# Kernel tuning notes

Measured on AMD Instinct MI355X. Metric: run time of the kernel, lower is better.

## Reference

```python
import jax, jax.numpy as jnp
import numpy as np
from jax import lax

GAIN = 16.0           # encoder_gains[0]
TEMP = 0.3            # soft_round_temperature
MASK = 9              # mask_size
PAD = 4               # (MASK - 1) // 2
# dim_arm = 16 causal taps inside the 9x9 mask (all indices < center index 40)
CTX_IDX = [12, 13, 14, 20, 21, 22, 23, 24, 28, 29, 30, 31, 32, 33, 38, 39]
CTX_OFF = [(i // MASK, i % MASK) for i in CTX_IDX]
IMG_H, IMG_W = 1024, 1536
N_GRIDS = 7
SIZES = [(int(np.ceil(IMG_H / 2 ** i)), int(np.ceil(IMG_W / 2 ** i))) for i in range(N_GRIDS)]
N_TOTAL = sum(h * w for h, w in SIZES)  # 2097024


def _softround(x, t):
    fl = jnp.floor(x)
    return fl + 0.5 * jnp.tanh((x - fl - 0.5) / t) / jnp.tanh(0.5 / t) + 0.5


def _forward(latents, noise_u, arm_w1, arm_b1, arm_w2, arm_b2, arm_wo, arm_bo,
             ups_k, pre_k, syn_w1, syn_b1, syn_w2, syn_b2):
    # --- quantize latents: softround(softround(x*g) + kumaraswamy noise), a=1 -> uniform-0.5 ---
    flat = jnp.concatenate([l.reshape(-1) for l in latents]) * GAIN
    flat_q = _softround(_softround(flat, TEMP) + (noise_u - 0.5), TEMP)
    dec, cnt = [], 0
    for h, w in SIZES:
        dec.append(flat_q[cnt:cnt + h * w].reshape(1, 1, h, w))
        cnt += h * w
    # --- _get_neighbor: masked causal context gather (16 taps of the 9x9 mask) ---
    ctxs = []
    for l in dec:
        h, w = l.shape[2], l.shape[3]
        xp = jnp.pad(l[0, 0], PAD)  # zero pad, matches F.pad constant 0
        ctxs.append(jnp.stack([xp[dy:dy + h, dx:dx + w] for dy, dx in CTX_OFF], axis=-1).reshape(-1, len(CTX_OFF)))
    ctx = jnp.concatenate(ctxs, axis=0)  # [N, 16]
    # --- ARM MLP: residual hidden layers, final linear to (mu, log_scale) ---
    h1 = jax.nn.relu(ctx @ arm_w1.T + arm_b1 + ctx)
    h2 = jax.nn.relu(h1 @ arm_w2.T + arm_b2 + h1)
    raw = h2 @ arm_wo.T + arm_bo
    mu, log_s = raw[:, 0], raw[:, 1]
    scale = jnp.exp(-0.5 * jnp.clip(log_s, -13.8155, 13.8155))
    def lcdf(x):
        return 0.5 - 0.5 * jnp.sign(x - mu) * jnp.expm1(-jnp.abs(x - mu) / scale)
    proba = jnp.maximum(lcdf(flat_q + 0.5) - lcdf(flat_q - 0.5), 2.0 ** -16)
    rate = -jnp.log2(proba)
    # --- upsampling: coarse-to-fine, depthwise separable convT x2 + preconcat filter ---
    x = dec[-1]
    for step, i in enumerate(range(N_GRIDS - 1, 0, -1)):
        c = x.shape[1]
        kern = jnp.broadcast_to(jnp.outer(ups_k[step], ups_k[step])[None, None], (c, 1, 8, 8))
        x = lax.conv_general_dilated(x, kern, (1, 1), ((4, 4), (4, 4)), lhs_dilation=(2, 2),
                                     dimension_numbers=('NCHW', 'OIHW', 'NCHW'), feature_group_count=c)
        ht, wt = SIZES[i - 1]
        x = x[:, :, :ht, :wt]
        pk2 = jnp.outer(pre_k[step], pre_k[step])[None, None]  # (1,1,7,7)
        t = lax.conv_general_dilated(dec[i - 1], pk2, (1, 1), ((3, 3), (3, 3)),
                                     dimension_numbers=('NCHW', 'OIHW', 'NCHW'))
        x = jnp.concatenate([t, x], axis=1)
    # --- synthesis: 1x1 conv 7->48 relu, 48->6, split mean / log_scale ---
    hid = jax.nn.relu(jnp.einsum('bchw,oc->bohw', x, syn_w1) + syn_b1[None, :, None, None])
    out = jnp.einsum('bchw,oc->bohw', hid, syn_w2) + syn_b2[None, :, None, None]
    pixel_mean, pixel_log_scale = out[:, :3], out[:, 3:]
    # F.interpolate to img_size is identity here (already full resolution)
    decoded = jnp.clip(pixel_mean, 0.0, 1.0)
    return pixel_mean, pixel_log_scale, decoded, rate


def setup_inputs():
    key = jax.random.key(0)
    ks = jax.random.split(key, 16)
    d = {}
    for i, (h, w) in enumerate(SIZES):
        d['latent%d' % i] = jax.random.uniform(ks[i], (1, 1, h, w), jnp.float32, -0.5, 0.5)
    d['noise_u'] = jax.random.uniform(ks[7], (N_TOTAL,), jnp.float32)
    d['arm_w1'] = jax.random.normal(ks[8], (16, 16), jnp.float32) * 0.25
    d['arm_b1'] = jnp.zeros((16,), jnp.float32)
    d['arm_w2'] = jax.random.normal(ks[9], (16, 16), jnp.float32) * 0.25
    d['arm_b2'] = jnp.zeros((16,), jnp.float32)
    d['arm_wo'] = jax.random.normal(ks[10], (2, 16), jnp.float32) * 0.25
    d['arm_bo'] = jnp.zeros((2,), jnp.float32)
    d['ups_k'] = jax.random.normal(ks[11], (6, 8), jnp.float32) * 0.2 + 0.125
    d['pre_k'] = jax.random.normal(ks[12], (6, 7), jnp.float32) * 0.2 + 0.1
    d['syn_w1'] = jax.random.normal(ks[13], (48, 7), jnp.float32) * 0.3
    d['syn_b1'] = jnp.zeros((48,), jnp.float32)
    d['syn_w2'] = jax.random.normal(ks[14], (6, 48), jnp.float32) * 0.1
    d['syn_b2'] = jnp.zeros((6,), jnp.float32)
    return d


def reference(latent0, latent1, latent2, latent3, latent4, latent5, latent6, noise_u,
              arm_w1, arm_b1, arm_w2, arm_b2, arm_wo, arm_bo,
              ups_k, pre_k, syn_w1, syn_b1, syn_w2, syn_b2):
    return _forward([latent0, latent1, latent2, latent3, latent4, latent5, latent6], noise_u,
                    arm_w1, arm_b1, arm_w2, arm_b2, arm_wo, arm_bo,
                    ups_k, pre_k, syn_w1, syn_b1, syn_w2, syn_b2)
```

## Files before the change

kernel.cpp:

```cpp
#include <hip/hip_runtime.h>
#include <math.h>

#define N_TOTAL 2097024
#define HWF (1024 * 1536)

#define OFF0 0
#define OFF1 1572864
#define OFF2 1966080
#define OFF3 2064384
#define OFF4 2088960
#define OFF5 2095104
#define OFF6 2096640

#define OUT_LS   (3 * HWF)
#define OUT_DEC  (6 * HWF)
#define OUT_RATE (9 * HWF)

typedef float f4 __attribute__((ext_vector_type(4), aligned(4)));
typedef float f2 __attribute__((ext_vector_type(2), aligned(4)));
typedef _Float16 h2 __attribute__((ext_vector_type(2)));
typedef __fp16 fp16v2 __attribute__((ext_vector_type(2)));

__device__ __forceinline__ h2 as_h2(unsigned u) {
    union { unsigned u; h2 h; } x; x.u = u; return x.h;
}
__device__ __forceinline__ h2 pkrtz(float a, float b) {
    union { fp16v2 f; h2 h; } x;
    x.f = __builtin_amdgcn_cvt_pkrtz(a, b);
    return x.h;
}
__device__ __forceinline__ float dot2f(h2 a, h2 b, float c) {
#if __has_builtin(__builtin_amdgcn_fdot2)
    return __builtin_amdgcn_fdot2(a, b, c, false);
#else
    return fmaf((float)a[0], (float)b[0], fmaf((float)a[1], (float)b[1], c));
#endif
}

__device__ __forceinline__ float softround_f(float x) {
    const float INV_T = 1.0f / 0.3f;
    const float HALF_OVER_TANH = 0.53699381f;
    float fl = floorf(x);
    float z = (x - fl - 0.5f) * INV_T;
    float e = __expf(2.0f * z);
    float th = 1.0f - 2.0f * __builtin_amdgcn_rcpf(e + 1.0f);
    return fl + th * HALF_OVER_TANH + 0.5f;
}

__global__ void pack_weights_kernel(const float* __restrict__ w1, const float* __restrict__ b1,
                                    const float* __restrict__ w2, unsigned* __restrict__ wp) {
    int t = threadIdx.x;
    if (t < 192) {
        int k = t >> 2, p = t & 3;
        float x = w1[k * 7 + 2 * p];
        float y = (p < 3) ? w1[k * 7 + 2 * p + 1] : b1[k];
        union { h2 h; unsigned u; } c;
        c.h = (h2){(_Float16)x, (_Float16)y};
        wp[t] = c.u;
    } else if (t < 336) {
        int r = t - 192;
        int o = r / 24, kk = r - o * 24;
        union { h2 h; unsigned u; } c;
        c.h = (h2){(_Float16)w2[o * 48 + 2 * kk], (_Float16)w2[o * 48 + 2 * kk + 1]};
        wp[t] = c.u;
    }
}

__global__ void quant_kernel(const float* __restrict__ l0, const float* __restrict__ l1,
                             const float* __restrict__ l2, const float* __restrict__ l3,
                             const float* __restrict__ l4, const float* __restrict__ l5,
                             const float* __restrict__ l6, const float* __restrict__ noise,
                             float* __restrict__ flat_q) {
    int idx = blockIdx.x * blockDim.x + threadIdx.x;
    if (idx >= N_TOTAL) return;
    float v;
    if      (idx < OFF1) v = l0[idx - OFF0];
    else if (idx < OFF2) v = l1[idx - OFF1];
    else if (idx < OFF3) v = l2[idx - OFF2];
    else if (idx < OFF4) v = l3[idx - OFF3];
    else if (idx < OFF5) v = l4[idx - OFF4];
    else if (idx < OFF6) v = l5[idx - OFF5];
    else                 v = l6[idx - OFF6];
    float x = v * 16.0f;
    float s1 = softround_f(x);
    float s2 = softround_f(s1 + noise[idx] - 0.5f);
    flat_q[idx] = s2;
}

template <int H, int W, int OFFT>
__device__ __forceinline__ void arm_body(const float* __restrict__ flat_q, int pos,
                                         const float* __restrict__ w1, const float* __restrict__ b1,
                                         const float* __restrict__ w2, const float* __restrict__ b2,
                                         const float* __restrict__ wo, const float* __restrict__ bo,
                                         float* __restrict__ rate_out) {
    if (pos >= H * W) return;
    unsigned up = (unsigned)pos;
    int y = up / (unsigned)W;
    int x = pos - y * W;
    const float* g = flat_q + OFFT + (size_t)y * W + x;

    float ctx[16];
    if (y >= 3 && x >= 3 && x <= W - 3) {
        f4 r3  = *(const f4*)(g - 3 * W - 1);
        f4 r2a = *(const f4*)(g - 2 * W - 2);
        float r2b = g[-2 * W + 2];
        f4 r1a = *(const f4*)(g - W - 3);
        f2 r1b = *(const f2*)(g - W + 1);
        f2 r0  = *(const f2*)(g - 2);
        ctx[0] = r3.x;  ctx[1] = r3.y;  ctx[2] = r3.z;
        ctx[3] = r2a.x; ctx[4] = r2a.y; ctx[5] = r2a.z; ctx[6] = r2a.w; ctx[7] = r2b;
        ctx[8] = r1a.x; ctx[9] = r1a.y; ctx[10] = r1a.z; ctx[11] = r1a.w;
        ctx[12] = r1b.x; ctx[13] = r1b.y;
        ctx[14] = r0.x; ctx[15] = r0.y;
    } else {
        const int DY[16] = {-3,-3,-3,-2,-2,-2,-2,-2,-1,-1,-1,-1,-1,-1, 0, 0};
        const int DX[16] = {-1, 0, 1,-2,-1, 0, 1, 2,-3,-2,-1, 0, 1, 2,-2,-1};
#pragma unroll
        for (int k = 0; k < 16; k++) {
            int yy = y + DY[k], xx = x + DX[k];
            ctx[k] = (yy >= 0 && yy < H && xx >= 0 && xx < W)
                         ? flat_q[OFFT + (size_t)yy * W + xx] : 0.0f;
        }
    }

    float h1[16];
#pragma unroll 4
    for (int j = 0; j < 16; j++) {
        float acc = b1[j] + ctx[j];
#pragma unroll
        for (int k = 0; k < 16; k++) acc = fmaf(w1[j * 16 + k], ctx[k], acc);
        h1[j] = fmaxf(acc, 0.0f);
    }
    float h2v[16];
#pragma unroll 4
    for (int j = 0; j < 16; j++) {
        float acc = b2[j] + h1[j];
#pragma unroll
        for (int k = 0; k < 16; k++) acc = fmaf(w2[j * 16 + k], h1[k], acc);
        h2v[j] = fmaxf(acc, 0.0f);
    }
    float mu = bo[0], ls = bo[1];
#pragma unroll
    for (int k = 0; k < 16; k++) {
        mu = fmaf(wo[k], h2v[k], mu);
        ls = fmaf(wo[16 + k], h2v[k], ls);
    }
    ls = fminf(fmaxf(ls, -13.8155f), 13.8155f);
    float inv_scale = __expf(0.5f * ls);

    float q = g[0];
    float da = (q + 0.5f) - mu;
    float db = (q - 0.5f) - mu;
    float ea = __expf(-fabsf(da) * inv_scale);
    float eb = __expf(-fabsf(db) * inv_scale);
    float la = 0.5f - 0.5f * copysignf(1.0f, da) * (ea - 1.0f);
    float lb = 0.5f - 0.5f * copysignf(1.0f, db) * (eb - 1.0f);
    float proba = fmaxf(la - lb, 1.52587890625e-05f);
    rate_out[OFFT + pos] = -__log2f(proba);
}

__global__ __launch_bounds__(256) void arm_all_kernel(
    const float* __restrict__ flat_q,
    const float* __restrict__ w1, const float* __restrict__ b1,
    const float* __restrict__ w2, const float* __restrict__ b2,
    const float* __restrict__ wo, const float* __restrict__ bo,
    float* __restrict__ rate_out) {
    int b = blockIdx.x;
    int t = threadIdx.x;
    if (b < 6144) {
        arm_body<1024, 1536, OFF0>(flat_q, b * 256 + t, w1, b1, w2, b2, wo, bo, rate_out);
    } else if (b < 7680) {
        arm_body<512, 768, OFF1>(flat_q, (b - 6144) * 256 + t, w1, b1, w2, b2, wo, bo, rate_out);
    } else if (b < 8064) {
        arm_body<256, 384, OFF2>(flat_q, (b - 7680) * 256 + t, w1, b1, w2, b2, wo, bo, rate_out);
    } else if (b < 8160) {
        arm_body<128, 192, OFF3>(flat_q, (b - 8064) * 256 + t, w1, b1, w2, b2, wo, bo, rate_out);
    } else if (b < 8184) {
        arm_body<64, 96, OFF4>(flat_q, (b - 8160) * 256 + t, w1, b1, w2, b2, wo, bo, rate_out);
    } else if (b < 8190) {
        arm_body<32, 48, OFF5>(flat_q, (b - 8184) * 256 + t, w1, b1, w2, b2, wo, bo, rate_out);
    } else {
        arm_body<16, 24, OFF6>(flat_q, (b - 8190) * 256 + t, w1, b1, w2, b2, wo, bo, rate_out);
    }
}

__device__ __forceinline__ void up_quad(const float* __restrict__ in, int H, int W,
                                        int i, int j, const float* K, float o[4]) {
    float w[5][5];
    bool interior = (i >= 2 && i <= H - 3 && j >= 2 && j <= W - 3);
    if (interior) {
        const float* p = in + (i - 2) * W + (j - 2);
#pragma unroll
        for (int r = 0; r < 5; r++) {
            f4 a = *(const f4*)p;
            w[r][0] = a.x; w[r][1] = a.y; w[r][2] = a.z; w[r][3] = a.w;
            w[r][4] = p[4];
            p += W;
        }
    } else {
#pragma unroll
        for (int r = 0; r < 5; r++)
#pragma unroll
            for (int e = 0; e < 5; e++) {
                int yy = i - 2 + r, xx = j - 2 + e;
                w[r][e] = (yy >= 0 && yy < H && xx >= 0 && xx < W) ? in[yy * W + xx] : 0.0f;
            }
    }
    float h0[5], h1[5];
#pragma unroll
    for (int r = 0; r < 5; r++) {
        h0[r] = K[0]*w[r][0] + K[2]*w[r][1] + K[4]*w[r][2] + K[6]*w[r][3];
        h1[r] = K[1]*w[r][1] + K[3]*w[r][2] + K[5]*w[r][3] + K[7]*w[r][4];
    }
    o[0] = K[0]*h0[0] + K[2]*h0[1] + K[4]*h0[2] + K[6]*h0[3];
    o[1] = K[0]*h1[0] + K[2]*h1[1] + K[4]*h1[2] + K[6]*h1[3];
    o[2] = K[1]*h0[1] + K[3]*h0[2] + K[5]*h0[3] + K[7]*h0[4];
    o[3] = K[1]*h1[1] + K[3]*h1[2] + K[5]*h1[3] + K[7]*h1[4];
}

__device__ __forceinline__ void conv7_quad(const float* __restrict__ dec, int H, int W,
                                           int i, int j, const float* k, float o[4]) {
    int Y = 2 * i, X = 2 * j;
    float g0[8], g1[8];
    bool interior = (Y - 3 >= 0 && Y + 4 <= H - 1 && X - 3 >= 0 && X + 4 <= W - 1);
    if (interior) {
        const float* p = dec + (Y - 3) * W + (X - 3);
#pragma unroll
        for (int r = 0; r < 8; r++) {
            f4 a = *(const f4*)p;
            f4 b = *(const f4*)(p + 4);
            g0[r] = k[0]*a.x + k[1]*a.y + k[2]*a.z + k[3]*a.w + k[4]*b.x + k[5]*b.y + k[6]*b.z;
            g1[r] = k[0]*a.y + k[1]*a.z + k[2]*a.w + k[3]*b.x + k[4]*b.y + k[5]*b.z + k[6]*b.w;
            p += W;
        }
    } else {
#pragma unroll
        for (int r = 0; r < 8; r++) {
            float wv[8];
#pragma unroll
            for (int q = 0; q < 8; q++) {
                int yy = Y - 3 + r, xx = X - 3 + q;
                wv[q] = (yy >= 0 && yy < H && xx >= 0 && xx < W) ? dec[yy * W + xx] : 0.0f;
            }
            g0[r] = k[0]*wv[0] + k[1]*wv[1] + k[2]*wv[2] + k[3]*wv[3] + k[4]*wv[4] + k[5]*wv[5] + k[6]*wv[6];
            g1[r] = k[0]*wv[1] + k[1]*wv[2] + k[2]*wv[3] + k[3]*wv[4] + k[4]*wv[5] + k[5]*wv[6] + k[6]*wv[7];
        }
    }
    o[0] = k[0]*g0[0] + k[1]*g0[1] + k[2]*g0[2] + k[3]*g0[3] + k[4]*g0[4] + k[5]*g0[5] + k[6]*g0[6];
    o[1] = k[0]*g1[0] + k[1]*g1[1] + k[2]*g1[2] + k[3]*g1[3] + k[4]*g1[4] + k[5]*g1[5] + k[6]*g1[6];
    o[2] = k[0]*g0[1] + k[1]*g0[2] + k[2]*g0[3] + k[3]*g0[4] + k[4]*g0[5] + k[5]*g0[6] + k[6]*g0[7];
    o[3] = k[0]*g1[1] + k[1]*g1[2] + k[2]*g1[3] + k[3]*g1[4] + k[4]*g1[5] + k[5]*g1[6] + k[6]*g1[7];
}

__global__ void pyramid_quad_kernel(const float* __restrict__ xin, int hin, int win_,
                                    const float* __restrict__ dec,
                                    const float* __restrict__ upsk, const float* __restrict__ prek,
                                    float* __restrict__ xout, int hout, int wout) {
    int qw = wout >> 1, qh = hout >> 1;
    int j = blockIdx.x * blockDim.x + threadIdx.x;
    int i = blockIdx.y * blockDim.y + threadIdx.y;
    int c = blockIdx.z;
    if (j >= qw || i >= qh) return;
    float o[4];
    if (c == 0) {
        float k[7];
#pragma unroll
        for (int p = 0; p < 7; p++) k[p] = prek[p];
        conv7_quad(dec, hout, wout, i, j, k, o);
    } else {
        float K[8];
#pragma unroll
        for (int p = 0; p < 8; p++) K[p] = upsk[p];
        up_quad(xin + (size_t)(c - 1) * hin * win_, hin, win_, i, j, K, o);
    }
    size_t base = ((size_t)c * hout + 2 * i) * wout + 2 * j;
    *(float2*)(xout + base)        = make_float2(o[0], o[1]);
    *(float2*)(xout + base + wout) = make_float2(o[2], o[3]);
}

__global__ __launch_bounds__(256) void final_kernel(
    const float* __restrict__ up_in,
    const float* __restrict__ dec0,
    const float* __restrict__ upsk, const float* __restrict__ prek,
    const unsigned* __restrict__ wp,
    const float* __restrict__ b2,
    float* __restrict__ out) {
    const int H2_ = 512, W2_ = 768, H1_ = 1024, W1_ = 1536;
    int t = threadIdx.x;
    int j = blockIdx.x * 16 + (t & 15);
    int i = blockIdx.y * 16 + (t >> 4);

    float K[8], kp[7];
#pragma unroll
    for (int p = 0; p < 8; p++) K[p] = upsk[p];
#pragma unroll
    for (int p = 0; p < 7; p++) kp[p] = prek[p];

    float px0[7], px1[7], px2[7], px3[7];
    {
        float o[4];
        conv7_quad(dec0, H1_, W1_, i, j, kp, o);
        px0[0] = o[0]; px1[0] = o[1]; px2[0] = o[2]; px3[0] = o[3];
    }
#pragma unroll
    for (int c = 0; c < 6; c++) {
        float o[4];
        up_quad(up_in + (size_t)c * (H2_ * W2_), H2_, W2_, i, j, K, o);
        px0[c + 1] = o[0]; px1[c + 1] = o[1]; px2[c + 1] = o[2]; px3[c + 1] = o[3];
    }

    h2 pp[4][4];
#pragma unroll
    for (int c = 0; c < 3; c++) {
        pp[0][c] = pkrtz(px0[2 * c], px0[2 * c + 1]);
        pp[1][c] = pkrtz(px1[2 * c], px1[2 * c + 1]);
        pp[2][c] = pkrtz(px2[2 * c], px2[2 * c + 1]);
        pp[3][c] = pkrtz(px3[2 * c], px3[2 * c + 1]);
    }
    pp[0][3] = pkrtz(px0[6], 1.0f);
    pp[1][3] = pkrtz(px1[6], 1.0f);
    pp[2][3] = pkrtz(px2[6], 1.0f);
    pp[3][3] = pkrtz(px3[6], 1.0f);

    float acc[6][4];
#pragma unroll
    for (int o = 0; o < 6; o++) {
        float b = b2[o];
#pragma unroll
        for (int q = 0; q < 4; q++) acc[o][q] = b;
    }
    const unsigned* w1p = wp;
    const unsigned* w2p = wp + 192;
#pragma unroll 4
    for (int kk = 0; kk < 24; kk++) {
        h2 wk0[4], wk1[4];
#pragma unroll
        for (int p = 0; p < 4; p++) {
            wk0[p] = as_h2(w1p[(2 * kk) * 4 + p]);
            wk1[p] = as_h2(w1p[(2 * kk + 1) * 4 + p]);
        }
        float a0[4], a1[4];
#pragma unroll
        for (int q = 0; q < 4; q++) {
            float s0 = 0.0f, s1 = 0.0f;
#pragma unroll
            for (int p = 0; p < 4; p++) {
                s0 = dot2f(wk0[p], pp[q][p], s0);
                s1 = dot2f(wk1[p], pp[q][p], s1);
            }
            a0[q] = fmaxf(s0, 0.0f);
            a1[q] = fmaxf(s1, 0.0f);
        }
        h2 hp[4];
#pragma unroll
        for (int q = 0; q < 4; q++)
            hp[q] = pkrtz(a0[q], a1[q]);
#pragma unroll
        for (int o = 0; o < 6; o++) {
            h2 w2k = as_h2(w2p[o * 24 + kk]);
#pragma unroll
            for (int q = 0; q < 4; q++)
                acc[o][q] = dot2f(w2k, hp[q], acc[o][q]);
        }
    }

    size_t base = (size_t)(2 * i) * W1_ + 2 * j;
#pragma unroll
    for (int c = 0; c < 3; c++) {
        *(float2*)(out + (size_t)c * HWF + base)       = make_float2(acc[c][0], acc[c][1]);
        *(float2*)(out + (size_t)c * HWF + base + W1_) = make_float2(acc[c][2], acc[c][3]);
        *(float2*)(out + OUT_LS + (size_t)c * HWF + base)       = make_float2(acc[c + 3][0], acc[c + 3][1]);
        *(float2*)(out + OUT_LS + (size_t)c * HWF + base + W1_) = make_float2(acc[c + 3][2], acc[c + 3][3]);
        *(float2*)(out + OUT_DEC + (size_t)c * HWF + base) =
            make_float2(fminf(fmaxf(acc[c][0], 0.0f), 1.0f), fminf(fmaxf(acc[c][1], 0.0f), 1.0f));
        *(float2*)(out + OUT_DEC + (size_t)c * HWF + base + W1_) =
            make_float2(fminf(fmaxf(acc[c][2], 0.0f), 1.0f), fminf(fmaxf(acc[c][3], 0.0f), 1.0f));
    }
}

extern "C" void kernel_launch(void* const* d_in, const int* in_sizes, int n_in,
                              void* d_out, int out_size, void* d_ws, size_t ws_size,
                              hipStream_t stream) {
    const float* lat[7];
    for (int i = 0; i < 7; i++) lat[i] = (const float*)d_in[i];
    const float* noise  = (const float*)d_in[7];
    const float* arm_w1 = (const float*)d_in[8];
    const float* arm_b1 = (const float*)d_in[9];
    const float* arm_w2 = (const float*)d_in[10];
    const float* arm_b2 = (const float*)d_in[11];
    const float* arm_wo = (const float*)d_in[12];
    const float* arm_bo = (const float*)d_in[13];
    const float* ups_k  = (const float*)d_in[14];
    const float* pre_k  = (const float*)d_in[15];
    const float* syn_w1 = (const float*)d_in[16];
    const float* syn_b1 = (const float*)d_in[17];
    const float* syn_w2 = (const float*)d_in[18];
    const float* syn_b2 = (const float*)d_in[19];
    float* out = (float*)d_out;

    float* flat_q = (float*)d_ws;
    float* bufA   = flat_q + N_TOTAL;
    float* bufB   = bufA + 6 * 512 * 768;
    unsigned* wpack = (unsigned*)(bufB + 5 * 256 * 384);

    static const int SH[7]  = {1024, 512, 256, 128, 64, 32, 16};
    static const int SW[7]  = {1536, 768, 384, 192, 96, 48, 24};
    static const int OFF[7] = {OFF0, OFF1, OFF2, OFF3, OFF4, OFF5, OFF6};

    pack_weights_kernel<<<1, 512, 0, stream>>>(syn_w1, syn_b1, syn_w2, wpack);

    quant_kernel<<<(N_TOTAL + 255) / 256, 256, 0, stream>>>(
        lat[0], lat[1], lat[2], lat[3], lat[4], lat[5], lat[6], noise, flat_q);

    arm_all_kernel<<<8192, 256, 0, stream>>>(flat_q, arm_w1, arm_b1, arm_w2, arm_b2,
                                             arm_wo, arm_bo, out + OUT_RATE);

    const float* xin = flat_q + OFF6;
    float* bufs[2] = {bufA, bufB};
    for (int s = 0; s < 5; s++) {
        int i    = 6 - s;
        int hin  = SH[i], win_ = SW[i];
        int hout = SH[i - 1], wout = SW[i - 1];
        float* xout = bufs[s & 1];
        dim3 blk(16, 16);
        dim3 grd((wout / 2 + 15) / 16, (hout / 2 + 15) / 16, s + 2);
        pyramid_quad_kernel<<<grd, blk, 0, stream>>>(xin, hin, win_,
                                                     flat_q + OFF[i - 1],
                                                     ups_k + s * 8, pre_k + s * 7,
                                                     xout, hout, wout);
        xin = xout;
    }

    dim3 fgrd(768 / 16, 512 / 16);
    final_kernel<<<fgrd, 256, 0, stream>>>(bufA, flat_q,
                                           ups_k + 5 * 8, pre_k + 5 * 7,
                                           wpack, syn_b2, out);
}
```

Before: 144.4 us.

## Vectorize quant kernel and remap final kernel to column-pair threads

The quant kernel now processes four elements per thread with 16-byte vector loads and stores. All level offsets are multiples of 4, so no vector straddles two latents. The final kernel changes each thread's work from a 2x2 output quad to a vertical pair at one full-resolution column. This gives fully coalesced scalar stores across a 64-wide row and vectorized separable conv and upsample reads on interior pixels. In exchange each thread reloads more overlapping input rows and does more redundant horizontal filtering, and the thread count doubles.

```diff
diff --git a/kernel.cpp b/kernel.cpp
--- a/kernel.cpp
+++ b/kernel.cpp
@@ -18,6 +18,7 @@
 
 typedef float f4 __attribute__((ext_vector_type(4), aligned(4)));
 typedef float f2 __attribute__((ext_vector_type(2), aligned(4)));
+typedef float f4a16 __attribute__((ext_vector_type(4), aligned(16)));
 typedef _Float16 h2 __attribute__((ext_vector_type(2)));
 typedef __fp16 fp16v2 __attribute__((ext_vector_type(2)));
 
@@ -71,20 +72,27 @@
                              const float* __restrict__ l4, const float* __restrict__ l5,
                              const float* __restrict__ l6, const float* __restrict__ noise,
                              float* __restrict__ flat_q) {
-    int idx = blockIdx.x * blockDim.x + threadIdx.x;
+    int idx = (blockIdx.x * 256 + threadIdx.x) * 4;
     if (idx >= N_TOTAL) return;
-    float v;
-    if      (idx < OFF1) v = l0[idx - OFF0];
-    else if (idx < OFF2) v = l1[idx - OFF1];
-    else if (idx < OFF3) v = l2[idx - OFF2];
-    else if (idx < OFF4) v = l3[idx - OFF3];
-    else if (idx < OFF5) v = l4[idx - OFF4];
-    else if (idx < OFF6) v = l5[idx - OFF5];
-    else                 v = l6[idx - OFF6];
-    float x = v * 16.0f;
-    float s1 = softround_f(x);
-    float s2 = softround_f(s1 + noise[idx] - 0.5f);
-    flat_q[idx] = s2;
+    const float* src;
+    int base;
+    if      (idx < OFF1) { src = l0; base = idx - OFF0; }
+    else if (idx < OFF2) { src = l1; base = idx - OFF1; }
+    else if (idx < OFF3) { src = l2; base = idx - OFF2; }
+    else if (idx < OFF4) { src = l3; base = idx - OFF3; }
+    else if (idx < OFF5) { src = l4; base = idx - OFF4; }
+    else if (idx < OFF6) { src = l5; base = idx - OFF5; }
+    else                 { src = l6; base = idx - OFF6; }
+    f4a16 v = *(const f4a16*)(src + base);
+    f4a16 n = *(const f4a16*)(noise + idx);
+    f4a16 r;
+#pragma unroll
+    for (int c = 0; c < 4; c++) {
+        float x = v[c] * 16.0f;
+        float s1 = softround_f(x);
+        r[c] = softround_f(s1 + n[c] - 0.5f);
+    }
+    *(f4a16*)(flat_q + idx) = r;
 }
 
 template <int H, int W, int OFFT>
@@ -287,8 +295,9 @@
     float* __restrict__ out) {
     const int H2_ = 512, W2_ = 768, H1_ = 1024, W1_ = 1536;
     int t = threadIdx.x;
-    int j = blockIdx.x * 16 + (t & 15);
-    int i = blockIdx.y * 16 + (t >> 4);
+    int X  = blockIdx.x * 64 + (t & 63);
+    int ip = blockIdx.y * 4 + (t >> 6);
+    int Y = 2 * ip;
 
     float K[8], kp[7];
 #pragma unroll
@@ -296,39 +305,98 @@
 #pragma unroll
     for (int p = 0; p < 7; p++) kp[p] = prek[p];
 
-    float px0[7], px1[7], px2[7], px3[7];
+    float pxe[7], pxo[7];
+
     {
-        float o[4];
-        conv7_quad(dec0, H1_, W1_, i, j, kp, o);
-        px0[0] = o[0]; px1[0] = o[1]; px2[0] = o[2]; px3[0] = o[3];
-    }
-#pragma unroll
-    for (int c = 0; c < 6; c++) {
-        float o[4];
-        up_quad(up_in + (size_t)c * (H2_ * W2_), H2_, W2_, i, j, K, o);
-        px0[c + 1] = o[0]; px1[c + 1] = o[1]; px2[c + 1] = o[2]; px3[c + 1] = o[3];
-    }
-
-    h2 pp[4][4];
+        float g[8];
+        bool interior = (Y >= 4 && Y <= H1_ - 6 && X >= 3 && X <= W1_ - 5);
+        if (interior) {
+            const float* p = dec0 + (size_t)(Y - 3) * W1_ + (X - 3);
+#pragma unroll
+            for (int r = 0; r < 8; r++) {
+                f4 a = *(const f4*)p;
+                f4 b = *(const f4*)(p + 4);
+                g[r] = kp[0]*a.x + kp[1]*a.y + kp[2]*a.z + kp[3]*a.w
+                     + kp[4]*b.x + kp[5]*b.y + kp[6]*b.z;
+                p += W1_;
+            }
+        } else {
+#pragma unroll
+            for (int r = 0; r < 8; r++) {
+                float s = 0.0f;
+#pragma unroll
+                for (int q = 0; q < 7; q++) {
+                    int yy = Y - 3 + r, xx = X - 3 + q;
+                    float v = (yy >= 0 && yy < H1_ && xx >= 0 && xx < W1_)
+                                  ? dec0[(size_t)yy * W1_ + xx] : 0.0f;
+                    s = fmaf(kp[q], v, s);
+                }
+                g[r] = s;
+            }
+        }
+        float oe = 0.0f, oo = 0.0f;
+#pragma unroll
+        for (int r = 0; r < 7; r++) {
+            oe = fmaf(kp[r], g[r], oe);
+            oo = fmaf(kp[r], g[r + 1], oo);
+        }
+        pxe[0] = oe; pxo[0] = oo;
+    }
+
+    {
+        int q0 = X & 1;
+        int j0 = (X >> 1) - 2 + q0;
+        float kh[4], kv0[4], kv1[4];
+#pragma unroll
+        for (int e = 0; e < 4; e++) {
+            kh[e]  = K[2 * e + q0];
+            kv0[e] = K[2 * e];
+            kv1[e] = K[2 * e + 1];
+        }
+        bool interior = (ip >= 2 && ip <= H2_ - 3 && j0 >= 0 && j0 + 3 < W2_);
+#pragma unroll
+        for (int c = 0; c < 6; c++) {
+            const float* base = up_in + (size_t)c * (H2_ * W2_);
+            float h[5];
+            if (interior) {
+                const float* p = base + (size_t)(ip - 2) * W2_ + j0;
+#pragma unroll
+                for (int r = 0; r < 5; r++) {
+                    f4 a = *(const f4*)p;
+                    h[r] = kh[0]*a.x + kh[1]*a.y + kh[2]*a.z + kh[3]*a.w;
+                    p += W2_;
+                }
+            } else {
+#pragma unroll
+                for (int r = 0; r < 5; r++) {
+                    float s = 0.0f;
+#pragma unroll
+                    for (int e = 0; e < 4; e++) {
+                        int yy = ip - 2 + r, xx = j0 + e;
+                        float v = (yy >= 0 && yy < H2_ && xx >= 0 && xx < W2_)
+                                      ? base[(size_t)yy * W2_ + xx] : 0.0f;
+                        s = fmaf(kh[e], v, s);
+                    }
+                    h[r] = s;
+                }
+            }
+            pxe[c + 1] = kv0[0]*h[0] + kv0[1]*h[1] + kv0[2]*h[2] + kv0[3]*h[3];
+            pxo[c + 1] = kv1[0]*h[1] + kv1[1]*h[2] + kv1[2]*h[3] + kv1[3]*h[4];
+        }
+    }
+
+    h2 ppe[4], ppo[4];
 #pragma unroll
     for (int c = 0; c < 3; c++) {
-        pp[0][c] = pkrtz(px0[2 * c], px0[2 * c + 1]);
-        pp[1][c] = pkrtz(px1[2 * c], px1[2 * c + 1]);
-        pp[2][c] = pkrtz(px2[2 * c], px2[2 * c + 1]);
-        pp[3][c] = pkrtz(px3[2 * c], px3[2 * c + 1]);
-    }
-    pp[0][3] = pkrtz(px0[6], 1.0f);
-    pp[1][3] = pkrtz(px1[6], 1.0f);
-    pp[2][3] = pkrtz(px2[6], 1.0f);
-    pp[3][3] = pkrtz(px3[6], 1.0f);
-
-    float acc[6][4];
-#pragma unroll
-    for (int o = 0; o < 6; o++) {
-        float b = b2[o];
-#pragma unroll
-        for (int q = 0; q < 4; q++) acc[o][q] = b;
-    }
+        ppe[c] = pkrtz(pxe[2 * c], pxe[2 * c + 1]);
+        ppo[c] = pkrtz(pxo[2 * c], pxo[2 * c + 1]);
+    }
+    ppe[3] = pkrtz(pxe[6], 1.0f);
+    ppo[3] = pkrtz(pxo[6], 1.0f);
+
+    float acce[6], acco[6];
+#pragma unroll
+    for (int o = 0; o < 6; o++) { acce[o] = b2[o]; acco[o] = b2[o]; }
     const unsigned* w1p = wp;
     const unsigned* w2p = wp + 192;
 #pragma unroll 4
@@ -339,42 +407,34 @@
             wk0[p] = as_h2(w1p[(2 * kk) * 4 + p]);
             wk1[p] = as_h2(w1p[(2 * kk + 1) * 4 + p]);
         }
-        float a0[4], a1[4];
-#pragma unroll
-        for (int q = 0; q < 4; q++) {
-            float s0 = 0.0f, s1 = 0.0f;
-#pragma unroll
-            for (int p = 0; p < 4; p++) {
-                s0 = dot2f(wk0[p], pp[q][p], s0);
-                s1 = dot2f(wk1[p], pp[q][p], s1);
-            }
-            a0[q] = fmaxf(s0, 0.0f);
-            a1[q] = fmaxf(s1, 0.0f);
-        }
-        h2 hp[4];
-#pragma unroll
-        for (int q = 0; q < 4; q++)
-            hp[q] = pkrtz(a0[q], a1[q]);
+        float s0e = 0.0f, s1e = 0.0f, s0o = 0.0f, s1o = 0.0f;
+#pragma unroll
+        for (int p = 0; p < 4; p++) {
+            s0e = dot2f(wk0[p], ppe[p], s0e);
+            s1e = dot2f(wk1[p], ppe[p], s1e);
+            s0o = dot2f(wk0[p], ppo[p], s0o);
+            s1o = dot2f(wk1[p], ppo[p], s1o);
+        }
+        h2 hpe = pkrtz(fmaxf(s0e, 0.0f), fmaxf(s1e, 0.0f));
+        h2 hpo = pkrtz(fmaxf(s0o, 0.0f), fmaxf(s1o, 0.0f));
 #pragma unroll
         for (int o = 0; o < 6; o++) {
             h2 w2k = as_h2(w2p[o * 24 + kk]);
-#pragma unroll
-            for (int q = 0; q < 4; q++)
-                acc[o][q] = dot2f(w2k, hp[q], acc[o][q]);
-        }
-    }
-
-    size_t base = (size_t)(2 * i) * W1_ + 2 * j;
+            acce[o] = dot2f(w2k, hpe, acce[o]);
+            acco[o] = dot2f(w2k, hpo, acco[o]);
+        }
+    }
+
+    size_t pe = (size_t)Y * W1_ + X;
+    size_t po = pe + W1_;
 #pragma unroll
     for (int c = 0; c < 3; c++) {
-        *(float2*)(out + (size_t)c * HWF + base)       = make_float2(acc[c][0], acc[c][1]);
-        *(float2*)(out + (size_t)c * HWF + base + W1_) = make_float2(acc[c][2], acc[c][3]);
-        *(float2*)(out + OUT_LS + (size_t)c * HWF + base)       = make_float2(acc[c + 3][0], acc[c + 3][1]);
-        *(float2*)(out + OUT_LS + (size_t)c * HWF + base + W1_) = make_float2(acc[c + 3][2], acc[c + 3][3]);
-        *(float2*)(out + OUT_DEC + (size_t)c * HWF + base) =
-            make_float2(fminf(fmaxf(acc[c][0], 0.0f), 1.0f), fminf(fmaxf(acc[c][1], 0.0f), 1.0f));
-        *(float2*)(out + OUT_DEC + (size_t)c * HWF + base + W1_) =
-            make_float2(fminf(fmaxf(acc[c][2], 0.0f), 1.0f), fminf(fmaxf(acc[c][3], 0.0f), 1.0f));
+        out[(size_t)c * HWF + pe] = acce[c];
+        out[(size_t)c * HWF + po] = acco[c];
+        out[OUT_LS + (size_t)c * HWF + pe] = acce[c + 3];
+        out[OUT_LS + (size_t)c * HWF + po] = acco[c + 3];
+        out[OUT_DEC + (size_t)c * HWF + pe] = fminf(fmaxf(acce[c], 0.0f), 1.0f);
+        out[OUT_DEC + (size_t)c * HWF + po] = fminf(fmaxf(acco[c], 0.0f), 1.0f);
     }
 }
 
@@ -409,7 +469,7 @@
 
     pack_weights_kernel<<<1, 512, 0, stream>>>(syn_w1, syn_b1, syn_w2, wpack);
 
-    quant_kernel<<<(N_TOTAL + 255) / 256, 256, 0, stream>>>(
+    quant_kernel<<<(N_TOTAL / 4 + 255) / 256, 256, 0, stream>>>(
         lat[0], lat[1], lat[2], lat[3], lat[4], lat[5], lat[6], noise, flat_q);
 
     arm_all_kernel<<<8192, 256, 0, stream>>>(flat_q, arm_w1, arm_b1, arm_w2, arm_b2,
@@ -431,7 +491,7 @@
         xin = xout;
     }
 
-    dim3 fgrd(768 / 16, 512 / 16);
+    dim3 fgrd(1536 / 64, 512 / 4);
     final_kernel<<<fgrd, 256, 0, stream>>>(bufA, flat_q,
                                            ups_k + 5 * 8, pre_k + 5 * 7,
                                            wpack, syn_b2, out);
```

New measurement: 139.7 us. 3.3% less time.
